# Kernel optimization log

Measured on AMD Instinct MI355X. Metric: run time of the kernel, lower is better.

Reference implementation:

```python
import jax, jax.numpy as jnp
import numpy as np

ITER_N = 5  # Newton-Schulz iterations (SqrtmLayer(cov, 5))


def covpool(x):
    # x: [B, C, M]. MPNCOV CovpoolLayer: x @ I_hat @ x^T with
    # I_hat = (1/M)(I - J/M), a projector, so cov = xc @ xc^T / M.
    M = x.shape[-1]
    xc = x - x.mean(axis=-1, keepdims=True)
    return jnp.einsum('bcm,bdm->bcd', xc, xc) / M


def sqrtm_ns(A, iter_n=ITER_N):
    # MPNCOV SqrtmLayer: trace-normalized Newton-Schulz matrix square root.
    C = A.shape[-1]
    I = jnp.eye(C, dtype=A.dtype)
    normA = jnp.trace(A, axis1=-2, axis2=-1)[:, None, None]  # [B,1,1]
    Y = A / normA
    Z = jnp.broadcast_to(I, A.shape)
    for i in range(iter_n):
        T = 0.5 * (3.0 * I - Z @ Y)
        Y_new = Y @ T
        if i < iter_n - 1:
            Z = T @ Z
        Y = Y_new
    return Y * jnp.sqrt(normA)


def setup_inputs() -> dict:
    key = jax.random.key(0)
    k1, k2, k3 = jax.random.split(key, 3)
    B, C, H, W = 32, 256, 64, 64
    r = 8
    x = jax.random.normal(k1, (B, C, H, W), dtype=jnp.float32)
    w1 = jax.random.normal(k2, (C // r, C), dtype=jnp.float32) * 0.05
    b1 = jnp.zeros((C // r,), dtype=jnp.float32)
    w2 = jax.random.normal(k3, (C, C // r), dtype=jnp.float32) * 0.05
    b2 = jnp.zeros((C,), dtype=jnp.float32)
    return {'x': x, 'w1': w1, 'b1': b1, 'w2': w2, 'b2': b2}


def reference(x, w1, b1, w2, b2):
    B, C, h, w = x.shape
    # h, w < 1000 => x_sub = x (no center crop)
    xf = x.reshape(B, C, h * w)
    cov = covpool(xf)                      # [B, C, C]
    cov_sqrt = sqrtm_ns(cov, ITER_N)       # [B, C, C]
    v = cov_sqrt.mean(axis=1)              # mean over dim 1 -> [B, C]
    # 1x1 convs on a 1x1 map == dense layers
    hdn = jax.nn.relu(jnp.einsum('oc,bc->bo', w1, v) + b1)
    a = jax.nn.sigmoid(jnp.einsum('oc,bc->bo', w2, hdn) + b2)  # [B, C]
    return a[:, :, None, None] * x
```

## Files before the change

kernel.cpp:

```cpp
#include <hip/hip_runtime.h>
#include <hip/hip_bf16.h>

typedef unsigned int uint32;
using short8 = __attribute__((ext_vector_type(8))) short;
using ushort4_t = __attribute__((ext_vector_type(4))) unsigned short;
using f32x4  = __attribute__((ext_vector_type(4))) float;

#define B_ 32
#define C_ 256
#define M_ 4096
#define MATF 2097152

#define AS1 __attribute__((address_space(1)))
#define AS3 __attribute__((address_space(3)))

__device__ inline ushort f2bf(float f) {
  uint32 u = __builtin_bit_cast(uint32, f);
  u += 0x7FFFu + ((u >> 16) & 1u);
  return (ushort)(u >> 16);
}
__device__ inline float bf2f(ushort u) {
  uint32 v = ((uint32)u) << 16;
  return __builtin_bit_cast(float, v);
}
__device__ inline void gl_lds16(const ushort* g, ushort* l) {
  __builtin_amdgcn_global_load_lds((const AS1 void*)g, (AS3 void*)l, 16, 0, 0);
}

__global__ __launch_bounds__(1024)
void covpool_kernel(const float* __restrict__ x, float* __restrict__ parts,
                    float* __restrict__ rs) {
  const int bid = blockIdx.x;
  const int b = bid >> 3, s = bid & 7;
  const int kb = s * 512;
  const float* Xb = x + (size_t)b * C_ * M_;
  float* P = parts + (size_t)s * MATF + ((size_t)b << 16);

  __shared__ ushort As[256 * 64];

  const int t    = threadIdx.x;
  const int lane = t & 63;
  const int w    = t >> 6;
  const int wr   = w >> 2, wc = w & 3;
  const int row  = t >> 2;
  const int ch   = t & 3;

  float rsum = 0.f;
  f32x4 acc[4][4];
#pragma unroll
  for (int m = 0; m < 4; ++m)
#pragma unroll
    for (int n = 0; n < 4; ++n) acc[m][n] = f32x4{0.f, 0.f, 0.f, 0.f};

  const int swzbase = (row & 7) << 4;
  char* wbase = (char*)As + row * 128;

  for (int k0 = kb; k0 < kb + 512; k0 += 64) {
    __syncthreads();
    const float* src = Xb + (size_t)row * M_ + k0 + ch * 16;
    const float4 v0 = ((const float4*)src)[0];
    const float4 v1 = ((const float4*)src)[1];
    const float4 v2 = ((const float4*)src)[2];
    const float4 v3 = ((const float4*)src)[3];
    rsum += v0.x + v0.y + v0.z + v0.w + v1.x + v1.y + v1.z + v1.w +
            v2.x + v2.y + v2.z + v2.w + v3.x + v3.y + v3.z + v3.w;
    short8 h0, h1;
    h0[0] = (short)f2bf(v0.x); h0[1] = (short)f2bf(v0.y);
    h0[2] = (short)f2bf(v0.z); h0[3] = (short)f2bf(v0.w);
    h0[4] = (short)f2bf(v1.x); h0[5] = (short)f2bf(v1.y);
    h0[6] = (short)f2bf(v1.z); h0[7] = (short)f2bf(v1.w);
    h1[0] = (short)f2bf(v2.x); h1[1] = (short)f2bf(v2.y);
    h1[2] = (short)f2bf(v2.z); h1[3] = (short)f2bf(v2.w);
    h1[4] = (short)f2bf(v3.x); h1[5] = (short)f2bf(v3.y);
    h1[6] = (short)f2bf(v3.z); h1[7] = (short)f2bf(v3.w);
    const int c0 = ch * 2;
    *(short8*)(wbase + ((c0 * 16) ^ swzbase))       = h0;
    *(short8*)(wbase + (((c0 + 1) * 16) ^ swzbase)) = h1;
    __syncthreads();
#pragma unroll
    for (int kk = 0; kk < 2; ++kk) {
      short8 af[4], bfr[4];
      const int slot = kk * 4 + (lane >> 4);
#pragma unroll
      for (int m = 0; m < 4; ++m) {
        const int ar = wr * 64 + m * 16 + (lane & 15);
        af[m] = *(const short8*)((const char*)As + ar * 128 + ((slot * 16) ^ ((ar & 7) << 4)));
      }
#pragma unroll
      for (int n = 0; n < 4; ++n) {
        const int br = wc * 64 + n * 16 + (lane & 15);
        bfr[n] = *(const short8*)((const char*)As + br * 128 + ((slot * 16) ^ ((br & 7) << 4)));
      }
#pragma unroll
      for (int m = 0; m < 4; ++m)
#pragma unroll
        for (int n = 0; n < 4; ++n)
          acc[m][n] = __builtin_amdgcn_mfma_f32_16x16x32_bf16(af[m], bfr[n], acc[m][n], 0, 0, 0);
    }
  }

  rsum += __shfl_xor(rsum, 1);
  rsum += __shfl_xor(rsum, 2);
  if (ch == 0) rs[b * 2048 + s * 256 + row] = rsum;

#pragma unroll
  for (int m = 0; m < 4; ++m)
#pragma unroll
    for (int n = 0; n < 4; ++n)
#pragma unroll
      for (int r = 0; r < 4; ++r) {
        const int lr = wr * 64 + m * 16 + ((lane >> 4) * 4) + r;
        const int lc = wc * 64 + n * 16 + (lane & 15);
        P[(size_t)lr * C_ + lc] = acc[m][n][r];
      }
}

__global__ __launch_bounds__(256)
void trace_kernel(const float* __restrict__ parts, const float* __restrict__ rs,
                  float* __restrict__ invn, float* __restrict__ sqrtn) {
  const int b = blockIdx.x;
  const int i = threadIdx.x;
  const float invM = 1.0f / (float)M_;
  float d = 0.f, m = 0.f;
#pragma unroll
  for (int s = 0; s < 8; ++s) {
    d += parts[(size_t)s * MATF + ((size_t)b << 16) + (size_t)i * 257];
    m += rs[b * 2048 + s * 256 + i];
  }
  const float mu = m * invM;
  float v = d * invM - mu * mu;
#pragma unroll
  for (int o = 32; o > 0; o >>= 1) v += __shfl_xor(v, o);
  __shared__ float wsum[4];
  if ((i & 63) == 0) wsum[i >> 6] = v;
  __syncthreads();
  if (i == 0) {
    const float n = wsum[0] + wsum[1] + wsum[2] + wsum[3];
    invn[b]  = 1.0f / n;
    sqrtn[b] = sqrtf(n);
  }
}

__global__ __launch_bounds__(256)
void reduceprep_kernel(const float* __restrict__ parts, const float* __restrict__ rs,
                       const float* __restrict__ invn,
                       ushort* __restrict__ Y0, ushort* __restrict__ Z1) {
  const int idx = blockIdx.x * 256 + threadIdx.x;
  const int b   = idx >> 14;
  const int rem = idx & 16383;
  const int i   = rem >> 6;
  const int j   = (rem & 63) * 4;
  const float invM = 1.0f / (float)M_;
  const float4* p4 = (const float4*)parts;

  float4 g = {0.f, 0.f, 0.f, 0.f};
  float  mi = 0.f;
  float4 mj = {0.f, 0.f, 0.f, 0.f};
#pragma unroll
  for (int s = 0; s < 8; ++s) {
    const float4 gs = p4[(size_t)s * (MATF / 4) + idx];
    g.x += gs.x; g.y += gs.y; g.z += gs.z; g.w += gs.w;
    const float* rrow = rs + b * 2048 + s * 256;
    mi += rrow[i];
    const float4 ms = *(const float4*)(rrow + j);
    mj.x += ms.x; mj.y += ms.y; mj.z += ms.z; mj.w += ms.w;
  }
  mi *= invM;
  const float in = invn[b];
  float y0 = (g.x * invM - mi * (mj.x * invM)) * in;
  float y1 = (g.y * invM - mi * (mj.y * invM)) * in;
  float y2 = (g.z * invM - mi * (mj.z * invM)) * in;
  float y3 = (g.w * invM - mi * (mj.w * invM)) * in;

  ushort4_t yv, zv;
  yv[0] = f2bf(y0); yv[1] = f2bf(y1); yv[2] = f2bf(y2); yv[3] = f2bf(y3);
  zv[0] = f2bf((j + 0 == i ? 1.5f : 0.f) - 0.5f * y0);
  zv[1] = f2bf((j + 1 == i ? 1.5f : 0.f) - 0.5f * y1);
  zv[2] = f2bf((j + 2 == i ? 1.5f : 0.f) - 0.5f * y2);
  zv[3] = f2bf((j + 3 == i ? 1.5f : 0.f) - 0.5f * y3);
  ((ushort4_t*)Y0)[idx] = yv;
  ((ushort4_t*)Z1)[idx] = zv;
}

#define MODE_T 0
#define MODE_W 1
#define MODE_I0 2

template <int MODE>
__global__ __launch_bounds__(256)
void gemm_ns(const ushort* __restrict__ A0, const ushort* __restrict__ A1,
             const ushort* __restrict__ Bm,
             ushort* __restrict__ O0, ushort* __restrict__ O1) {
  const int bid0 = blockIdx.x;
  int bid = (MODE == MODE_W) ? ((bid0 & 7) * 128 + (bid0 >> 3))
                             : ((bid0 & 7) * 64 + (bid0 >> 3));
  const ushort* Aall = A0;
  ushort* Oall = O0;
  if (MODE == MODE_W && bid >= 512) { bid -= 512; Aall = A1; Oall = O1; }
  const int b    = bid >> 4;
  const int tile = bid & 15;
  const int rb   = (tile >> 2) * 64;
  const int cb   = (tile & 3) * 64;
  const ushort* Ap = Aall + ((size_t)b << 16) + rb * C_;
  const ushort* Bp = Bm   + ((size_t)b << 16) + cb * C_;
  ushort* Op = Oall + ((size_t)b << 16);

  __shared__ ushort As[64 * 64];
  __shared__ ushort Bs[64 * 64];

  const int t    = threadIdx.x;
  const int lane = t & 63;
  const int wid  = t >> 6;
  const int wr   = wid >> 1, wc = wid & 1;

  const int srow0 = t >> 3;
  const int sc0   = (t & 7) ^ (srow0 & 7);
  const int srow1 = 32 + srow0;
  const int sc1   = (t & 7) ^ (srow1 & 7);

  f32x4 acc[2][2];
#pragma unroll
  for (int m = 0; m < 2; ++m)
#pragma unroll
    for (int n = 0; n < 2; ++n) acc[m][n] = f32x4{0.f, 0.f, 0.f, 0.f};

  for (int k0 = 0; k0 < C_; k0 += 64) {
    __syncthreads();
    gl_lds16(Ap + (size_t)srow0 * C_ + k0 + sc0 * 8, (ushort*)((char*)As + wid * 1024));
    gl_lds16(Ap + (size_t)srow1 * C_ + k0 + sc1 * 8, (ushort*)((char*)As + 4096 + wid * 1024));
    gl_lds16(Bp + (size_t)srow0 * C_ + k0 + sc0 * 8, (ushort*)((char*)Bs + wid * 1024));
    gl_lds16(Bp + (size_t)srow1 * C_ + k0 + sc1 * 8, (ushort*)((char*)Bs + 4096 + wid * 1024));
    __syncthreads();
#pragma unroll
    for (int kk = 0; kk < 2; ++kk) {
      short8 af[2], bfr[2];
      const int slot = kk * 4 + (lane >> 4);
#pragma unroll
      for (int m = 0; m < 2; ++m) {
        const int ar = wr * 32 + m * 16 + (lane & 15);
        af[m] = *(const short8*)((const char*)As + ar * 128 + ((slot * 16) ^ ((ar & 7) << 4)));
      }
#pragma unroll
      for (int n = 0; n < 2; ++n) {
        const int br = wc * 32 + n * 16 + (lane & 15);
        bfr[n] = *(const short8*)((const char*)Bs + br * 128 + ((slot * 16) ^ ((br & 7) << 4)));
      }
#pragma unroll
      for (int m = 0; m < 2; ++m)
#pragma unroll
        for (int n = 0; n < 2; ++n)
          acc[m][n] = __builtin_amdgcn_mfma_f32_16x16x32_bf16(af[m], bfr[n], acc[m][n], 0, 0, 0);
    }
  }

#pragma unroll
  for (int m = 0; m < 2; ++m)
#pragma unroll
    for (int n = 0; n < 2; ++n)
#pragma unroll
      for (int r = 0; r < 4; ++r) {
        const int lr = wr * 32 + m * 16 + ((lane >> 4) * 4) + r;
        const int lc = wc * 32 + n * 16 + (lane & 15);
        const float v = acc[m][n][r];
        float o;
        if (MODE == MODE_T)       o = (((rb + lr) == (cb + lc)) ? 1.5f : 0.0f) - 0.5f * v;
        else if (MODE == MODE_W)  o = v;
        else         o = 1.5f * bf2f(Ap[lr * C_ + (cb + lc)]) - 0.5f * v;
        Op[(size_t)(rb + lr) * C_ + (cb + lc)] = f2bf(o);
      }
}

__global__ __launch_bounds__(256)
void final_kernel(const ushort* __restrict__ Y, const ushort* __restrict__ T,
                  const float* __restrict__ sqrtn,
                  const float* __restrict__ w1, const float* __restrict__ b1,
                  const float* __restrict__ w2, const float* __restrict__ b2,
                  float* __restrict__ a) {
  const int b = blockIdx.x;
  const int c = threadIdx.x;
  __shared__ float u[C_], vv[C_], h[32];
  const ushort* Yb = Y + ((size_t)b << 16);
  const ushort* Tb = T + ((size_t)b << 16);

  float s = 0.f;
  for (int i = 0; i < C_; ++i) s += bf2f(Yb[(size_t)i * C_ + c]);
  u[c] = s * (1.0f / (float)C_);
  __syncthreads();

  float acc = 0.f;
  for (int k = 0; k < C_; ++k) acc += u[k] * bf2f(Tb[(size_t)k * C_ + c]);
  vv[c] = acc * sqrtn[b];
  __syncthreads();

  if (c < 32) {
    float hh = b1[c];
    for (int k = 0; k < C_; ++k) hh += w1[c * C_ + k] * vv[k];
    h[c] = fmaxf(hh, 0.0f);
  }
  __syncthreads();

  float aa = b2[c];
#pragma unroll
  for (int o = 0; o < 32; ++o) aa += w2[c * 32 + o] * h[o];
  a[b * C_ + c] = 1.0f / (1.0f + expf(-aa));
}

__global__ __launch_bounds__(256)
void scale_kernel(const float* __restrict__ x, const float* __restrict__ a,
                  float* __restrict__ out) {
  const int stride = gridDim.x * blockDim.x;
  const int n4 = B_ * C_ * M_ / 4;
  for (int i = blockIdx.x * blockDim.x + threadIdx.x; i < n4; i += stride) {
    const float4 v = ((const float4*)x)[i];
    const float s = a[i >> 10];
    float4 o = { v.x * s, v.y * s, v.z * s, v.w * s };
    ((float4*)out)[i] = o;
  }
}

extern "C" void kernel_launch(void* const* d_in, const int* in_sizes, int n_in,
                              void* d_out, int out_size, void* d_ws, size_t ws_size,
                              hipStream_t stream) {
  const float* x  = (const float*)d_in[0];
  const float* w1 = (const float*)d_in[1];
  const float* b1 = (const float*)d_in[2];
  const float* w2 = (const float*)d_in[3];
  const float* b2 = (const float*)d_in[4];
  float* out = (float*)d_out;

  float* ws = (float*)d_ws;
  float* parts = ws;
  float* rs    = ws + 8 * (size_t)MATF;
  float* invn  = rs + 65536;
  float* sqrtn = invn + 32;
  float* a     = sqrtn + 32;
  ushort* bfb  = (ushort*)(a + 8192);
  ushort* Yb0  = bfb;
  ushort* Yb1  = bfb + 1 * (size_t)MATF;
  ushort* Zb0  = bfb + 2 * (size_t)MATF;
  ushort* Zb1  = bfb + 3 * (size_t)MATF;
  ushort* Tb   = bfb + 4 * (size_t)MATF;

  covpool_kernel<<<256, 1024, 0, stream>>>(x, parts, rs);
  trace_kernel<<<32, 256, 0, stream>>>(parts, rs, invn, sqrtn);
  reduceprep_kernel<<<2048, 256, 0, stream>>>(parts, rs, invn, Yb0, Zb0);

  gemm_ns<MODE_I0><<<512, 256, 0, stream>>>(Yb0, nullptr, Yb0, Yb1, nullptr);
  gemm_ns<MODE_T><<<512, 256, 0, stream>>>(Zb0, nullptr, Yb1, Tb, nullptr);
  gemm_ns<MODE_W><<<1024, 256, 0, stream>>>(Yb1, Zb0, Tb, Yb0, Zb1);
  gemm_ns<MODE_T><<<512, 256, 0, stream>>>(Zb1, nullptr, Yb0, Tb, nullptr);
  gemm_ns<MODE_W><<<1024, 256, 0, stream>>>(Yb0, Zb1, Tb, Yb1, Zb0);
  gemm_ns<MODE_T><<<512, 256, 0, stream>>>(Zb0, nullptr, Yb1, Tb, nullptr);
  gemm_ns<MODE_W><<<1024, 256, 0, stream>>>(Yb1, Zb0, Tb, Yb0, Zb1);
  gemm_ns<MODE_T><<<512, 256, 0, stream>>>(Zb1, nullptr, Yb0, Tb, nullptr);

  final_kernel<<<32, 256, 0, stream>>>(Yb0, Tb, sqrtn, w1, b1, w2, b2, a);
  scale_kernel<<<4096, 256, 0, stream>>>(x, a, out);
}
```

Baseline: 367.9 us.

## Reformulate Newton-Schulz via commuting polynomial in normalized covariance and mean vector

The Newton-Schulz iteration is rewritten using the fact that Y and Z are polynomials of the normalized covariance A. Only one matrix E_k is updated, E_{k+1} = E_k(1.5I - 0.5E_k^2), through two GEMM launches per step. The column mean is carried as a vector via matrix-vector products fused into the same launches, which removes the separate T, W and Z GEMMs and the associated memory traffic. The change also stores covariance partial sums as bf16 instead of fp32, cutting the split-K reduction traffic, and double-buffers the LDS stages in both the covpool and GEMM kernels. It adds bf16 rounding error on the partial sums and relies on the commuting-polynomial identity staying numerically close to the reference.

```diff
diff --git a/kernel.cpp b/kernel.cpp
--- a/kernel.cpp
+++ b/kernel.cpp
@@ -15,9 +15,8 @@
 #define AS3 __attribute__((address_space(3)))
 
 __device__ inline ushort f2bf(float f) {
-  uint32 u = __builtin_bit_cast(uint32, f);
-  u += 0x7FFFu + ((u >> 16) & 1u);
-  return (ushort)(u >> 16);
+  __hip_bfloat16 h = __float2bfloat16(f);
+  return __builtin_bit_cast(unsigned short, h);
 }
 __device__ inline float bf2f(ushort u) {
   uint32 v = ((uint32)u) << 16;
@@ -28,15 +27,15 @@
 }
 
 __global__ __launch_bounds__(1024)
-void covpool_kernel(const float* __restrict__ x, float* __restrict__ parts,
+void covpool_kernel(const float* __restrict__ x, ushort* __restrict__ parts,
                     float* __restrict__ rs) {
   const int bid = blockIdx.x;
   const int b = bid >> 3, s = bid & 7;
   const int kb = s * 512;
   const float* Xb = x + (size_t)b * C_ * M_;
-  float* P = parts + (size_t)s * MATF + ((size_t)b << 16);
-
-  __shared__ ushort As[256 * 64];
+  ushort* P = parts + (size_t)s * MATF + ((size_t)b << 16);
+
+  __shared__ ushort As[2][256 * 64];
 
   const int t    = threadIdx.x;
   const int lane = t & 63;
@@ -53,30 +52,35 @@
     for (int n = 0; n < 4; ++n) acc[m][n] = f32x4{0.f, 0.f, 0.f, 0.f};
 
   const int swzbase = (row & 7) << 4;
-  char* wbase = (char*)As + row * 128;
-
-  for (int k0 = kb; k0 < kb + 512; k0 += 64) {
+  const float* srcbase = Xb + (size_t)row * M_ + ch * 16;
+
+  float4 cv[4];
+  {
+    const float4* p = (const float4*)(srcbase + kb);
+    cv[0] = p[0]; cv[1] = p[1]; cv[2] = p[2]; cv[3] = p[3];
+  }
+
+#pragma unroll
+  for (int st = 0; st < 8; ++st) {
+    float4 nv[4];
+    if (st < 7) {
+      const float4* p = (const float4*)(srcbase + kb + (st + 1) * 64);
+      nv[0] = p[0]; nv[1] = p[1]; nv[2] = p[2]; nv[3] = p[3];
+    }
+    char* wbase = (char*)As[st & 1] + row * 128;
+#pragma unroll
+    for (int q = 0; q < 2; ++q) {
+      const float4 a = cv[2 * q], bq = cv[2 * q + 1];
+      rsum += a.x + a.y + a.z + a.w + bq.x + bq.y + bq.z + bq.w;
+      short8 h;
+      h[0] = (short)f2bf(a.x);  h[1] = (short)f2bf(a.y);
+      h[2] = (short)f2bf(a.z);  h[3] = (short)f2bf(a.w);
+      h[4] = (short)f2bf(bq.x); h[5] = (short)f2bf(bq.y);
+      h[6] = (short)f2bf(bq.z); h[7] = (short)f2bf(bq.w);
+      *(short8*)(wbase + (((ch * 2 + q) * 16) ^ swzbase)) = h;
+    }
     __syncthreads();
-    const float* src = Xb + (size_t)row * M_ + k0 + ch * 16;
-    const float4 v0 = ((const float4*)src)[0];
-    const float4 v1 = ((const float4*)src)[1];
-    const float4 v2 = ((const float4*)src)[2];
-    const float4 v3 = ((const float4*)src)[3];
-    rsum += v0.x + v0.y + v0.z + v0.w + v1.x + v1.y + v1.z + v1.w +
-            v2.x + v2.y + v2.z + v2.w + v3.x + v3.y + v3.z + v3.w;
-    short8 h0, h1;
-    h0[0] = (short)f2bf(v0.x); h0[1] = (short)f2bf(v0.y);
-    h0[2] = (short)f2bf(v0.z); h0[3] = (short)f2bf(v0.w);
-    h0[4] = (short)f2bf(v1.x); h0[5] = (short)f2bf(v1.y);
-    h0[6] = (short)f2bf(v1.z); h0[7] = (short)f2bf(v1.w);
-    h1[0] = (short)f2bf(v2.x); h1[1] = (short)f2bf(v2.y);
-    h1[2] = (short)f2bf(v2.z); h1[3] = (short)f2bf(v2.w);
-    h1[4] = (short)f2bf(v3.x); h1[5] = (short)f2bf(v3.y);
-    h1[6] = (short)f2bf(v3.z); h1[7] = (short)f2bf(v3.w);
-    const int c0 = ch * 2;
-    *(short8*)(wbase + ((c0 * 16) ^ swzbase))       = h0;
-    *(short8*)(wbase + (((c0 + 1) * 16) ^ swzbase)) = h1;
-    __syncthreads();
+    const char* rb_ = (const char*)As[st & 1];
 #pragma unroll
     for (int kk = 0; kk < 2; ++kk) {
       short8 af[4], bfr[4];
@@ -84,12 +88,12 @@
 #pragma unroll
       for (int m = 0; m < 4; ++m) {
         const int ar = wr * 64 + m * 16 + (lane & 15);
-        af[m] = *(const short8*)((const char*)As + ar * 128 + ((slot * 16) ^ ((ar & 7) << 4)));
+        af[m] = *(const short8*)(rb_ + ar * 128 + ((slot * 16) ^ ((ar & 7) << 4)));
       }
 #pragma unroll
       for (int n = 0; n < 4; ++n) {
         const int br = wc * 64 + n * 16 + (lane & 15);
-        bfr[n] = *(const short8*)((const char*)As + br * 128 + ((slot * 16) ^ ((br & 7) << 4)));
+        bfr[n] = *(const short8*)(rb_ + br * 128 + ((slot * 16) ^ ((br & 7) << 4)));
       }
 #pragma unroll
       for (int m = 0; m < 4; ++m)
@@ -97,6 +101,7 @@
         for (int n = 0; n < 4; ++n)
           acc[m][n] = __builtin_amdgcn_mfma_f32_16x16x32_bf16(af[m], bfr[n], acc[m][n], 0, 0, 0);
     }
+    if (st < 7) { cv[0] = nv[0]; cv[1] = nv[1]; cv[2] = nv[2]; cv[3] = nv[3]; }
   }
 
   rsum += __shfl_xor(rsum, 1);
@@ -111,12 +116,12 @@
       for (int r = 0; r < 4; ++r) {
         const int lr = wr * 64 + m * 16 + ((lane >> 4) * 4) + r;
         const int lc = wc * 64 + n * 16 + (lane & 15);
-        P[(size_t)lr * C_ + lc] = acc[m][n][r];
+        P[(size_t)lr * C_ + lc] = f2bf(acc[m][n][r]);
       }
 }
 
 __global__ __launch_bounds__(256)
-void trace_kernel(const float* __restrict__ parts, const float* __restrict__ rs,
+void trace_kernel(const ushort* __restrict__ parts, const float* __restrict__ rs,
                   float* __restrict__ invn, float* __restrict__ sqrtn) {
   const int b = blockIdx.x;
   const int i = threadIdx.x;
@@ -124,7 +129,7 @@
   float d = 0.f, m = 0.f;
 #pragma unroll
   for (int s = 0; s < 8; ++s) {
-    d += parts[(size_t)s * MATF + ((size_t)b << 16) + (size_t)i * 257];
+    d += bf2f(parts[(size_t)s * MATF + ((size_t)b << 16) + (size_t)i * 257]);
     m += rs[b * 2048 + s * 256 + i];
   }
   const float mu = m * invM;
@@ -142,24 +147,23 @@
 }
 
 __global__ __launch_bounds__(256)
-void reduceprep_kernel(const float* __restrict__ parts, const float* __restrict__ rs,
-                       const float* __restrict__ invn,
-                       ushort* __restrict__ Y0, ushort* __restrict__ Z1) {
+void reduceprep_kernel(const ushort* __restrict__ parts, const float* __restrict__ rs,
+                       const float* __restrict__ invn, ushort* __restrict__ E0) {
   const int idx = blockIdx.x * 256 + threadIdx.x;
   const int b   = idx >> 14;
   const int rem = idx & 16383;
   const int i   = rem >> 6;
   const int j   = (rem & 63) * 4;
   const float invM = 1.0f / (float)M_;
-  const float4* p4 = (const float4*)parts;
-
-  float4 g = {0.f, 0.f, 0.f, 0.f};
-  float  mi = 0.f;
+  const ushort4_t* p4 = (const ushort4_t*)parts;
+
+  float g0 = 0.f, g1 = 0.f, g2 = 0.f, g3 = 0.f;
+  float mi = 0.f;
   float4 mj = {0.f, 0.f, 0.f, 0.f};
 #pragma unroll
   for (int s = 0; s < 8; ++s) {
-    const float4 gs = p4[(size_t)s * (MATF / 4) + idx];
-    g.x += gs.x; g.y += gs.y; g.z += gs.z; g.w += gs.w;
+    const ushort4_t gs = p4[(size_t)s * (MATF / 4) + idx];
+    g0 += bf2f(gs[0]); g1 += bf2f(gs[1]); g2 += bf2f(gs[2]); g3 += bf2f(gs[3]);
     const float* rrow = rs + b * 2048 + s * 256;
     mi += rrow[i];
     const float4 ms = *(const float4*)(rrow + j);
@@ -167,46 +171,45 @@
   }
   mi *= invM;
   const float in = invn[b];
-  float y0 = (g.x * invM - mi * (mj.x * invM)) * in;
-  float y1 = (g.y * invM - mi * (mj.y * invM)) * in;
-  float y2 = (g.z * invM - mi * (mj.z * invM)) * in;
-  float y3 = (g.w * invM - mi * (mj.w * invM)) * in;
-
-  ushort4_t yv, zv;
-  yv[0] = f2bf(y0); yv[1] = f2bf(y1); yv[2] = f2bf(y2); yv[3] = f2bf(y3);
-  zv[0] = f2bf((j + 0 == i ? 1.5f : 0.f) - 0.5f * y0);
-  zv[1] = f2bf((j + 1 == i ? 1.5f : 0.f) - 0.5f * y1);
-  zv[2] = f2bf((j + 2 == i ? 1.5f : 0.f) - 0.5f * y2);
-  zv[3] = f2bf((j + 3 == i ? 1.5f : 0.f) - 0.5f * y3);
-  ((ushort4_t*)Y0)[idx] = yv;
-  ((ushort4_t*)Z1)[idx] = zv;
-}
-
-#define MODE_T 0
-#define MODE_W 1
-#define MODE_I0 2
-
-template <int MODE>
-__global__ __launch_bounds__(256)
-void gemm_ns(const ushort* __restrict__ A0, const ushort* __restrict__ A1,
-             const ushort* __restrict__ Bm,
-             ushort* __restrict__ O0, ushort* __restrict__ O1) {
+  ushort4_t ev;
+  ev[0] = f2bf((g0 * invM - mi * (mj.x * invM)) * in);
+  ev[1] = f2bf((g1 * invM - mi * (mj.y * invM)) * in);
+  ev[2] = f2bf((g2 * invM - mi * (mj.z * invM)) * in);
+  ev[3] = f2bf((g3 * invM - mi * (mj.w * invM)) * in);
+  ((ushort4_t*)E0)[idx] = ev;
+}
+
+template <int MV>
+__global__ __launch_bounds__(256)
+void gemm_i0(const ushort* __restrict__ A, const ushort* __restrict__ B,
+             ushort* __restrict__ O,
+             const float* __restrict__ win, float* __restrict__ wout) {
   const int bid0 = blockIdx.x;
-  int bid = (MODE == MODE_W) ? ((bid0 & 7) * 128 + (bid0 >> 3))
-                             : ((bid0 & 7) * 64 + (bid0 >> 3));
-  const ushort* Aall = A0;
-  ushort* Oall = O0;
-  if (MODE == MODE_W && bid >= 512) { bid -= 512; Aall = A1; Oall = O1; }
+  if (MV && bid0 >= 512) {
+    const int b = bid0 - 512;
+    const int t = threadIdx.x;
+    const ushort* Eb = B + ((size_t)b << 16);
+    __shared__ float wsm[256];
+    wsm[t] = win ? win[b * 256 + t] : (1.0f / 256.0f);
+    __syncthreads();
+    float acc = 0.f;
+#pragma unroll 4
+    for (int k = 0; k < 256; ++k) acc += bf2f(Eb[(size_t)k * 256 + t]) * wsm[k];
+    wout[b * 256 + t] = 1.5f * wsm[t] - 0.5f * acc;
+    return;
+  }
+
+  const int bid = (bid0 & 7) * 64 + (bid0 >> 3);
   const int b    = bid >> 4;
   const int tile = bid & 15;
   const int rb   = (tile >> 2) * 64;
   const int cb   = (tile & 3) * 64;
-  const ushort* Ap = Aall + ((size_t)b << 16) + rb * C_;
-  const ushort* Bp = Bm   + ((size_t)b << 16) + cb * C_;
-  ushort* Op = Oall + ((size_t)b << 16);
-
-  __shared__ ushort As[64 * 64];
-  __shared__ ushort Bs[64 * 64];
+  const ushort* Ap = A + ((size_t)b << 16) + rb * C_;
+  const ushort* Bp = B + ((size_t)b << 16) + cb * C_;
+  ushort* Op = O + ((size_t)b << 16);
+
+  __shared__ ushort As[2][64 * 64];
+  __shared__ ushort Bs[2][64 * 64];
 
   const int t    = threadIdx.x;
   const int lane = t & 63;
@@ -224,34 +227,53 @@
 #pragma unroll
     for (int n = 0; n < 2; ++n) acc[m][n] = f32x4{0.f, 0.f, 0.f, 0.f};
 
-  for (int k0 = 0; k0 < C_; k0 += 64) {
+#define STAGE(k0, c)                                                            \
+  do {                                                                          \
+    gl_lds16(Ap + (size_t)srow0 * C_ + (k0) + sc0 * 8, &As[c][0]    + wid*512); \
+    gl_lds16(Ap + (size_t)srow1 * C_ + (k0) + sc1 * 8, &As[c][2048] + wid*512); \
+    gl_lds16(Bp + (size_t)srow0 * C_ + (k0) + sc0 * 8, &Bs[c][0]    + wid*512); \
+    gl_lds16(Bp + (size_t)srow1 * C_ + (k0) + sc1 * 8, &Bs[c][2048] + wid*512); \
+  } while (0)
+
+#define COMPUTE(c)                                                              \
+  do {                                                                          \
+    const char* ab = (const char*)As[c];                                        \
+    const char* bb = (const char*)Bs[c];                                        \
+    _Pragma("unroll")                                                           \
+    for (int kk = 0; kk < 2; ++kk) {                                            \
+      short8 af[2], bfr[2];                                                     \
+      const int slot = kk * 4 + (lane >> 4);                                    \
+      _Pragma("unroll")                                                         \
+      for (int m = 0; m < 2; ++m) {                                             \
+        const int ar = wr * 32 + m * 16 + (lane & 15);                          \
+        af[m] = *(const short8*)(ab + ar * 128 + ((slot * 16) ^ ((ar & 7) << 4))); \
+      }                                                                         \
+      _Pragma("unroll")                                                         \
+      for (int n = 0; n < 2; ++n) {                                             \
+        const int br = wc * 32 + n * 16 + (lane & 15);                          \
+        bfr[n] = *(const short8*)(bb + br * 128 + ((slot * 16) ^ ((br & 7) << 4))); \
+      }                                                                         \
+      _Pragma("unroll")                                                         \
+      for (int m = 0; m < 2; ++m)                                               \
+        _Pragma("unroll")                                                       \
+        for (int n = 0; n < 2; ++n)                                             \
+          acc[m][n] = __builtin_amdgcn_mfma_f32_16x16x32_bf16(af[m], bfr[n], acc[m][n], 0, 0, 0); \
+    }                                                                           \
+  } while (0)
+
+  STAGE(0, 0);
+  __syncthreads();
+  int cur = 0;
+#pragma unroll
+  for (int k0 = 64; k0 < 256; k0 += 64) {
+    STAGE(k0, cur ^ 1);
+    COMPUTE(cur);
     __syncthreads();
-    gl_lds16(Ap + (size_t)srow0 * C_ + k0 + sc0 * 8, (ushort*)((char*)As + wid * 1024));
-    gl_lds16(Ap + (size_t)srow1 * C_ + k0 + sc1 * 8, (ushort*)((char*)As + 4096 + wid * 1024));
-    gl_lds16(Bp + (size_t)srow0 * C_ + k0 + sc0 * 8, (ushort*)((char*)Bs + wid * 1024));
-    gl_lds16(Bp + (size_t)srow1 * C_ + k0 + sc1 * 8, (ushort*)((char*)Bs + 4096 + wid * 1024));
-    __syncthreads();
-#pragma unroll
-    for (int kk = 0; kk < 2; ++kk) {
-      short8 af[2], bfr[2];
-      const int slot = kk * 4 + (lane >> 4);
-#pragma unroll
-      for (int m = 0; m < 2; ++m) {
-        const int ar = wr * 32 + m * 16 + (lane & 15);
-        af[m] = *(const short8*)((const char*)As + ar * 128 + ((slot * 16) ^ ((ar & 7) << 4)));
-      }
-#pragma unroll
-      for (int n = 0; n < 2; ++n) {
-        const int br = wc * 32 + n * 16 + (lane & 15);
-        bfr[n] = *(const short8*)((const char*)Bs + br * 128 + ((slot * 16) ^ ((br & 7) << 4)));
-      }
-#pragma unroll
-      for (int m = 0; m < 2; ++m)
-#pragma unroll
-        for (int n = 0; n < 2; ++n)
-          acc[m][n] = __builtin_amdgcn_mfma_f32_16x16x32_bf16(af[m], bfr[n], acc[m][n], 0, 0, 0);
-    }
-  }
+    cur ^= 1;
+  }
+  COMPUTE(cur);
+#undef STAGE
+#undef COMPUTE
 
 #pragma unroll
   for (int m = 0; m < 2; ++m)
@@ -261,35 +283,35 @@
       for (int r = 0; r < 4; ++r) {
         const int lr = wr * 32 + m * 16 + ((lane >> 4) * 4) + r;
         const int lc = wc * 32 + n * 16 + (lane & 15);
-        const float v = acc[m][n][r];
-        float o;
-        if (MODE == MODE_T)       o = (((rb + lr) == (cb + lc)) ? 1.5f : 0.0f) - 0.5f * v;
-        else if (MODE == MODE_W)  o = v;
-        else         o = 1.5f * bf2f(Ap[lr * C_ + (cb + lc)]) - 0.5f * v;
+        const float o = 1.5f * bf2f(Ap[lr * C_ + (cb + lc)]) - 0.5f * acc[m][n][r];
         Op[(size_t)(rb + lr) * C_ + (cb + lc)] = f2bf(o);
       }
 }
 
 __global__ __launch_bounds__(256)
-void final_kernel(const ushort* __restrict__ Y, const ushort* __restrict__ T,
-                  const float* __restrict__ sqrtn,
+void final_kernel(const ushort* __restrict__ E4, const ushort* __restrict__ E0,
+                  const float* __restrict__ wvin, const float* __restrict__ sqrtn,
                   const float* __restrict__ w1, const float* __restrict__ b1,
                   const float* __restrict__ w2, const float* __restrict__ b2,
                   float* __restrict__ a) {
   const int b = blockIdx.x;
   const int c = threadIdx.x;
-  __shared__ float u[C_], vv[C_], h[32];
-  const ushort* Yb = Y + ((size_t)b << 16);
-  const ushort* Tb = T + ((size_t)b << 16);
-
-  float s = 0.f;
-  for (int i = 0; i < C_; ++i) s += bf2f(Yb[(size_t)i * C_ + c]);
-  u[c] = s * (1.0f / (float)C_);
-  __syncthreads();
-
+  __shared__ float w4s[C_], w5[C_], vv[C_], h[32];
+  const ushort* E4b = E4 + ((size_t)b << 16);
+  const ushort* E0b = E0 + ((size_t)b << 16);
+
+  w4s[c] = wvin[b * C_ + c];
+  __syncthreads();
   float acc = 0.f;
-  for (int k = 0; k < C_; ++k) acc += u[k] * bf2f(Tb[(size_t)k * C_ + c]);
-  vv[c] = acc * sqrtn[b];
+#pragma unroll 4
+  for (int k = 0; k < C_; ++k) acc += bf2f(E4b[(size_t)k * C_ + c]) * w4s[k];
+  w5[c] = 1.5f * w4s[c] - 0.5f * acc;
+  __syncthreads();
+
+  float acc2 = 0.f;
+#pragma unroll 4
+  for (int k = 0; k < C_; ++k) acc2 += bf2f(E0b[(size_t)k * C_ + c]) * w5[k];
+  vv[c] = acc2 * sqrtn[b];
   __syncthreads();
 
   if (c < 32) {
@@ -329,31 +351,31 @@
   float* out = (float*)d_out;
 
   float* ws = (float*)d_ws;
-  float* parts = ws;
-  float* rs    = ws + 8 * (size_t)MATF;
+  ushort* partsbf = (ushort*)ws;
+  float* rs    = ws + 4 * (size_t)MATF;
   float* invn  = rs + 65536;
   float* sqrtn = invn + 32;
   float* a     = sqrtn + 32;
-  ushort* bfb  = (ushort*)(a + 8192);
-  ushort* Yb0  = bfb;
-  ushort* Yb1  = bfb + 1 * (size_t)MATF;
-  ushort* Zb0  = bfb + 2 * (size_t)MATF;
-  ushort* Zb1  = bfb + 3 * (size_t)MATF;
-  ushort* Tb   = bfb + 4 * (size_t)MATF;
-
-  covpool_kernel<<<256, 1024, 0, stream>>>(x, parts, rs);
-  trace_kernel<<<32, 256, 0, stream>>>(parts, rs, invn, sqrtn);
-  reduceprep_kernel<<<2048, 256, 0, stream>>>(parts, rs, invn, Yb0, Zb0);
-
-  gemm_ns<MODE_I0><<<512, 256, 0, stream>>>(Yb0, nullptr, Yb0, Yb1, nullptr);
-  gemm_ns<MODE_T><<<512, 256, 0, stream>>>(Zb0, nullptr, Yb1, Tb, nullptr);
-  gemm_ns<MODE_W><<<1024, 256, 0, stream>>>(Yb1, Zb0, Tb, Yb0, Zb1);
-  gemm_ns<MODE_T><<<512, 256, 0, stream>>>(Zb1, nullptr, Yb0, Tb, nullptr);
-  gemm_ns<MODE_W><<<1024, 256, 0, stream>>>(Yb0, Zb1, Tb, Yb1, Zb0);
-  gemm_ns<MODE_T><<<512, 256, 0, stream>>>(Zb0, nullptr, Yb1, Tb, nullptr);
-  gemm_ns<MODE_W><<<1024, 256, 0, stream>>>(Yb1, Zb0, Tb, Yb0, Zb1);
-  gemm_ns<MODE_T><<<512, 256, 0, stream>>>(Zb1, nullptr, Yb0, Tb, nullptr);
-
-  final_kernel<<<32, 256, 0, stream>>>(Yb0, Tb, sqrtn, w1, b1, w2, b2, a);
+  float* wvA   = a + 8192;
+  float* wvB   = wvA + 8192;
+  ushort* E0 = (ushort*)(wvB + 8192);
+  ushort* EB = E0 + (size_t)MATF;
+  ushort* EC = EB + (size_t)MATF;
+  ushort* U  = EC + (size_t)MATF;
+
+  covpool_kernel<<<256, 1024, 0, stream>>>(x, partsbf, rs);
+  trace_kernel<<<32, 256, 0, stream>>>(partsbf, rs, invn, sqrtn);
+  reduceprep_kernel<<<2048, 256, 0, stream>>>(partsbf, rs, invn, E0);
+
+  gemm_i0<1><<<544, 256, 0, stream>>>(E0, E0, U, nullptr, wvA);
+  gemm_i0<0><<<512, 256, 0, stream>>>(U, E0, EB, nullptr, nullptr);
+  gemm_i0<1><<<544, 256, 0, stream>>>(EB, EB, U, wvA, wvB);
+  gemm_i0<0><<<512, 256, 0, stream>>>(U, EB, EC, nullptr, nullptr);
+  gemm_i0<1><<<544, 256, 0, stream>>>(EC, EC, U, wvB, wvA);
+  gemm_i0<0><<<512, 256, 0, stream>>>(U, EC, EB, nullptr, nullptr);
+  gemm_i0<1><<<544, 256, 0, stream>>>(EB, EB, U, wvA, wvB);
+  gemm_i0<0><<<512, 256, 0, stream>>>(U, EB, EC, nullptr, nullptr);
+
+  final_kernel<<<32, 256, 0, stream>>>(EC, E0, wvB, sqrtn, w1, b1, w2, b2, a);
   scale_kernel<<<4096, 256, 0, stream>>>(x, a, out);
 }
```

Measured after the change: 445.8 us. 1.21x slower.

## Fuse Newton-Schulz iterations into one per-batch kernel using a symmetric recurrence

Applied to the files above, without the earlier changes.

Replaces the eight separate Y/Z/T GEMM launches and the final kernel with one kernel that runs one block per batch. It tracks a single symmetric matrix iterate and carries the column-mean vector through matrix-vector updates instead of keeping both Y and Z. The GEMMs now load MFMA operands straight from global memory, with no LDS staging. This removes launch overhead and halves the matrix state, but only 32 workgroups do all the matmul work, so GPU utilisation may fall sharply. The bf16 rounding path also changes to the library conversion.

```diff
diff --git a/kernel.cpp b/kernel.cpp
--- a/kernel.cpp
+++ b/kernel.cpp
@@ -11,20 +11,13 @@
 #define M_ 4096
 #define MATF 2097152
 
-#define AS1 __attribute__((address_space(1)))
-#define AS3 __attribute__((address_space(3)))
-
 __device__ inline ushort f2bf(float f) {
-  uint32 u = __builtin_bit_cast(uint32, f);
-  u += 0x7FFFu + ((u >> 16) & 1u);
-  return (ushort)(u >> 16);
+  __hip_bfloat16 h = __float2bfloat16(f);
+  return __builtin_bit_cast(unsigned short, h);
 }
 __device__ inline float bf2f(ushort u) {
   uint32 v = ((uint32)u) << 16;
   return __builtin_bit_cast(float, v);
-}
-__device__ inline void gl_lds16(const ushort* g, ushort* l) {
-  __builtin_amdgcn_global_load_lds((const AS1 void*)g, (AS3 void*)l, 16, 0, 0);
 }
 
 __global__ __launch_bounds__(1024)
@@ -143,8 +136,7 @@
 
 __global__ __launch_bounds__(256)
 void reduceprep_kernel(const float* __restrict__ parts, const float* __restrict__ rs,
-                       const float* __restrict__ invn,
-                       ushort* __restrict__ Y0, ushort* __restrict__ Z1) {
+                       const float* __restrict__ invn, ushort* __restrict__ E0) {
   const int idx = blockIdx.x * 256 + threadIdx.x;
   const int b   = idx >> 14;
   const int rem = idx & 16383;
@@ -167,142 +159,138 @@
   }
   mi *= invM;
   const float in = invn[b];
-  float y0 = (g.x * invM - mi * (mj.x * invM)) * in;
-  float y1 = (g.y * invM - mi * (mj.y * invM)) * in;
-  float y2 = (g.z * invM - mi * (mj.z * invM)) * in;
-  float y3 = (g.w * invM - mi * (mj.w * invM)) * in;
-
-  ushort4_t yv, zv;
-  yv[0] = f2bf(y0); yv[1] = f2bf(y1); yv[2] = f2bf(y2); yv[3] = f2bf(y3);
-  zv[0] = f2bf((j + 0 == i ? 1.5f : 0.f) - 0.5f * y0);
-  zv[1] = f2bf((j + 1 == i ? 1.5f : 0.f) - 0.5f * y1);
-  zv[2] = f2bf((j + 2 == i ? 1.5f : 0.f) - 0.5f * y2);
-  zv[3] = f2bf((j + 3 == i ? 1.5f : 0.f) - 0.5f * y3);
-  ((ushort4_t*)Y0)[idx] = yv;
-  ((ushort4_t*)Z1)[idx] = zv;
-}
-
-#define MODE_T 0
-#define MODE_W 1
-#define MODE_I0 2
-
-template <int MODE>
-__global__ __launch_bounds__(256)
-void gemm_ns(const ushort* __restrict__ A0, const ushort* __restrict__ A1,
-             const ushort* __restrict__ Bm,
-             ushort* __restrict__ O0, ushort* __restrict__ O1) {
-  const int bid0 = blockIdx.x;
-  int bid = (MODE == MODE_W) ? ((bid0 & 7) * 128 + (bid0 >> 3))
-                             : ((bid0 & 7) * 64 + (bid0 >> 3));
-  const ushort* Aall = A0;
-  ushort* Oall = O0;
-  if (MODE == MODE_W && bid >= 512) { bid -= 512; Aall = A1; Oall = O1; }
-  const int b    = bid >> 4;
-  const int tile = bid & 15;
-  const int rb   = (tile >> 2) * 64;
-  const int cb   = (tile & 3) * 64;
-  const ushort* Ap = Aall + ((size_t)b << 16) + rb * C_;
-  const ushort* Bp = Bm   + ((size_t)b << 16) + cb * C_;
-  ushort* Op = Oall + ((size_t)b << 16);
-
-  __shared__ ushort As[64 * 64];
-  __shared__ ushort Bs[64 * 64];
+  ushort4_t ev;
+  ev[0] = f2bf((g.x * invM - mi * (mj.x * invM)) * in);
+  ev[1] = f2bf((g.y * invM - mi * (mj.y * invM)) * in);
+  ev[2] = f2bf((g.z * invM - mi * (mj.z * invM)) * in);
+  ev[3] = f2bf((g.w * invM - mi * (mj.w * invM)) * in);
+  ((ushort4_t*)E0)[idx] = ev;
+}
+
+__device__ __forceinline__ void mm_unit(const ushort* __restrict__ Ap,
+                                        const ushort* __restrict__ Bp,
+                                        ushort* __restrict__ Op,
+                                        int R, int Cc, int lane) {
+  f32x4 acc[4][4];
+#pragma unroll
+  for (int m = 0; m < 4; ++m)
+#pragma unroll
+    for (int n = 0; n < 4; ++n) acc[m][n] = f32x4{0.f, 0.f, 0.f, 0.f};
+
+#pragma unroll 1
+  for (int ks = 0; ks < 8; ++ks) {
+    const int ko = ks * 32 + (lane >> 4) * 8;
+    short8 af[4], bfm[4];
+#pragma unroll
+    for (int m = 0; m < 4; ++m)
+      af[m] = *(const short8*)(Ap + (size_t)(R + m * 16 + (lane & 15)) * 256 + ko);
+#pragma unroll
+    for (int n = 0; n < 4; ++n)
+      bfm[n] = *(const short8*)(Bp + (size_t)(Cc + n * 16 + (lane & 15)) * 256 + ko);
+#pragma unroll
+    for (int m = 0; m < 4; ++m)
+#pragma unroll
+      for (int n = 0; n < 4; ++n)
+        acc[m][n] = __builtin_amdgcn_mfma_f32_16x16x32_bf16(af[m], bfm[n], acc[m][n], 0, 0, 0);
+  }
+
+#pragma unroll
+  for (int m = 0; m < 4; ++m)
+#pragma unroll
+    for (int n = 0; n < 4; ++n)
+#pragma unroll
+      for (int r = 0; r < 4; ++r) {
+        const int lr = R + m * 16 + ((lane >> 4) * 4) + r;
+        const int lc = Cc + n * 16 + (lane & 15);
+        const float o = 1.5f * bf2f(Ap[(size_t)lr * 256 + lc]) - 0.5f * acc[m][n][r];
+        Op[(size_t)lr * 256 + lc] = f2bf(o);
+      }
+}
+
+__global__ __launch_bounds__(1024)
+void ns_kernel(const ushort* __restrict__ E0g, ushort* __restrict__ Eag,
+               ushort* __restrict__ Ebg, ushort* __restrict__ Ug,
+               const float* __restrict__ sqrtn,
+               const float* __restrict__ w1, const float* __restrict__ b1,
+               const float* __restrict__ w2, const float* __restrict__ b2,
+               float* __restrict__ a) {
+  const int b = blockIdx.x;
+  const size_t off = (size_t)b << 16;
+  const ushort* E0 = E0g + off;
+  ushort* Ea = Eag + off;
+  ushort* Eb = Ebg + off;
+  ushort* U  = Ug  + off;
 
   const int t    = threadIdx.x;
   const int lane = t & 63;
-  const int wid  = t >> 6;
-  const int wr   = wid >> 1, wc = wid & 1;
-
-  const int srow0 = t >> 3;
-  const int sc0   = (t & 7) ^ (srow0 & 7);
-  const int srow1 = 32 + srow0;
-  const int sc1   = (t & 7) ^ (srow1 & 7);
-
-  f32x4 acc[2][2];
-#pragma unroll
-  for (int m = 0; m < 2; ++m)
-#pragma unroll
-    for (int n = 0; n < 2; ++n) acc[m][n] = f32x4{0.f, 0.f, 0.f, 0.f};
-
-  for (int k0 = 0; k0 < C_; k0 += 64) {
+  const int w    = t >> 6;
+  const int R    = (w >> 2) * 64;
+  const int Cc   = (w & 3) * 64;
+  const int c    = t & 255;
+  const int q    = t >> 8;
+
+  __shared__ float wv[2][C_];
+  __shared__ float pw[4][C_];
+  __shared__ float vv[C_];
+  __shared__ float hh[32];
+
+  if (t < C_) { wv[0][t] = 1.0f / (float)C_; }
+  __syncthreads();
+
+  const ushort* Ecur = E0;
+  int p = 0;
+#pragma unroll 1
+  for (int k = 0; k < 5; ++k) {
+    {
+      float part = 0.f;
+      const int k0 = q * 64;
+#pragma unroll 8
+      for (int kk = 0; kk < 64; ++kk)
+        part += bf2f(Ecur[(size_t)(k0 + kk) * C_ + c]) * wv[p][k0 + kk];
+      pw[q][c] = part;
+      __syncthreads();
+      if (t < C_) {
+        const float s = pw[0][t] + pw[1][t] + pw[2][t] + pw[3][t];
+        wv[p ^ 1][t] = 1.5f * wv[p][t] - 0.5f * s;
+      }
+      __syncthreads();
+      p ^= 1;
+    }
+    if (k < 4) {
+      mm_unit(Ecur, Ecur, U, R, Cc, lane);
+      __syncthreads();
+      ushort* Enext = (k & 1) ? Eb : Ea;
+      mm_unit(U, Ecur, Enext, R, Cc, lane);
+      __syncthreads();
+      Ecur = Enext;
+    }
+  }
+
+  {
+    float part = 0.f;
+    const int k0 = q * 64;
+#pragma unroll 8
+    for (int kk = 0; kk < 64; ++kk)
+      part += bf2f(E0[(size_t)(k0 + kk) * C_ + c]) * wv[p][k0 + kk];
+    pw[q][c] = part;
     __syncthreads();
-    gl_lds16(Ap + (size_t)srow0 * C_ + k0 + sc0 * 8, (ushort*)((char*)As + wid * 1024));
-    gl_lds16(Ap + (size_t)srow1 * C_ + k0 + sc1 * 8, (ushort*)((char*)As + 4096 + wid * 1024));
-    gl_lds16(Bp + (size_t)srow0 * C_ + k0 + sc0 * 8, (ushort*)((char*)Bs + wid * 1024));
-    gl_lds16(Bp + (size_t)srow1 * C_ + k0 + sc1 * 8, (ushort*)((char*)Bs + 4096 + wid * 1024));
+    if (t < C_)
+      vv[t] = (pw[0][t] + pw[1][t] + pw[2][t] + pw[3][t]) * sqrtn[b];
     __syncthreads();
-#pragma unroll
-    for (int kk = 0; kk < 2; ++kk) {
-      short8 af[2], bfr[2];
-      const int slot = kk * 4 + (lane >> 4);
-#pragma unroll
-      for (int m = 0; m < 2; ++m) {
-        const int ar = wr * 32 + m * 16 + (lane & 15);
-        af[m] = *(const short8*)((const char*)As + ar * 128 + ((slot * 16) ^ ((ar & 7) << 4)));
-      }
-#pragma unroll
-      for (int n = 0; n < 2; ++n) {
-        const int br = wc * 32 + n * 16 + (lane & 15);
-        bfr[n] = *(const short8*)((const char*)Bs + br * 128 + ((slot * 16) ^ ((br & 7) << 4)));
-      }
-#pragma unroll
-      for (int m = 0; m < 2; ++m)
-#pragma unroll
-        for (int n = 0; n < 2; ++n)
-          acc[m][n] = __builtin_amdgcn_mfma_f32_16x16x32_bf16(af[m], bfr[n], acc[m][n], 0, 0, 0);
-    }
-  }
-
-#pragma unroll
-  for (int m = 0; m < 2; ++m)
-#pragma unroll
-    for (int n = 0; n < 2; ++n)
-#pragma unroll
-      for (int r = 0; r < 4; ++r) {
-        const int lr = wr * 32 + m * 16 + ((lane >> 4) * 4) + r;
-        const int lc = wc * 32 + n * 16 + (lane & 15);
-        const float v = acc[m][n][r];
-        float o;
-        if (MODE == MODE_T)       o = (((rb + lr) == (cb + lc)) ? 1.5f : 0.0f) - 0.5f * v;
-        else if (MODE == MODE_W)  o = v;
-        else         o = 1.5f * bf2f(Ap[lr * C_ + (cb + lc)]) - 0.5f * v;
-        Op[(size_t)(rb + lr) * C_ + (cb + lc)] = f2bf(o);
-      }
-}
-
-__global__ __launch_bounds__(256)
-void final_kernel(const ushort* __restrict__ Y, const ushort* __restrict__ T,
-                  const float* __restrict__ sqrtn,
-                  const float* __restrict__ w1, const float* __restrict__ b1,
-                  const float* __restrict__ w2, const float* __restrict__ b2,
-                  float* __restrict__ a) {
-  const int b = blockIdx.x;
-  const int c = threadIdx.x;
-  __shared__ float u[C_], vv[C_], h[32];
-  const ushort* Yb = Y + ((size_t)b << 16);
-  const ushort* Tb = T + ((size_t)b << 16);
-
-  float s = 0.f;
-  for (int i = 0; i < C_; ++i) s += bf2f(Yb[(size_t)i * C_ + c]);
-  u[c] = s * (1.0f / (float)C_);
+  }
+
+  if (t < 32) {
+    float h = b1[t];
+    for (int k = 0; k < C_; ++k) h += w1[t * C_ + k] * vv[k];
+    hh[t] = fmaxf(h, 0.0f);
+  }
   __syncthreads();
-
-  float acc = 0.f;
-  for (int k = 0; k < C_; ++k) acc += u[k] * bf2f(Tb[(size_t)k * C_ + c]);
-  vv[c] = acc * sqrtn[b];
-  __syncthreads();
-
-  if (c < 32) {
-    float hh = b1[c];
-    for (int k = 0; k < C_; ++k) hh += w1[c * C_ + k] * vv[k];
-    h[c] = fmaxf(hh, 0.0f);
-  }
-  __syncthreads();
-
-  float aa = b2[c];
-#pragma unroll
-  for (int o = 0; o < 32; ++o) aa += w2[c * 32 + o] * h[o];
-  a[b * C_ + c] = 1.0f / (1.0f + expf(-aa));
+  if (t < C_) {
+    float aa = b2[t];
+#pragma unroll
+    for (int o = 0; o < 32; ++o) aa += w2[t * 32 + o] * hh[o];
+    a[b * C_ + t] = 1.0f / (1.0f + expf(-aa));
+  }
 }
 
 __global__ __launch_bounds__(256)
@@ -334,26 +322,14 @@
   float* invn  = rs + 65536;
   float* sqrtn = invn + 32;
   float* a     = sqrtn + 32;
-  ushort* bfb  = (ushort*)(a + 8192);
-  ushort* Yb0  = bfb;
-  ushort* Yb1  = bfb + 1 * (size_t)MATF;
-  ushort* Zb0  = bfb + 2 * (size_t)MATF;
-  ushort* Zb1  = bfb + 3 * (size_t)MATF;
-  ushort* Tb   = bfb + 4 * (size_t)MATF;
+  ushort* E0 = (ushort*)(a + 8192);
+  ushort* Ea = E0 + (size_t)MATF;
+  ushort* Eb = Ea + (size_t)MATF;
+  ushort* U  = Eb + (size_t)MATF;
 
   covpool_kernel<<<256, 1024, 0, stream>>>(x, parts, rs);
   trace_kernel<<<32, 256, 0, stream>>>(parts, rs, invn, sqrtn);
-  reduceprep_kernel<<<2048, 256, 0, stream>>>(parts, rs, invn, Yb0, Zb0);
-
-  gemm_ns<MODE_I0><<<512, 256, 0, stream>>>(Yb0, nullptr, Yb0, Yb1, nullptr);
-  gemm_ns<MODE_T><<<512, 256, 0, stream>>>(Zb0, nullptr, Yb1, Tb, nullptr);
-  gemm_ns<MODE_W><<<1024, 256, 0, stream>>>(Yb1, Zb0, Tb, Yb0, Zb1);
-  gemm_ns<MODE_T><<<512, 256, 0, stream>>>(Zb1, nullptr, Yb0, Tb, nullptr);
-  gemm_ns<MODE_W><<<1024, 256, 0, stream>>>(Yb0, Zb1, Tb, Yb1, Zb0);
-  gemm_ns<MODE_T><<<512, 256, 0, stream>>>(Zb0, nullptr, Yb1, Tb, nullptr);
-  gemm_ns<MODE_W><<<1024, 256, 0, stream>>>(Yb1, Zb0, Tb, Yb0, Zb1);
-  gemm_ns<MODE_T><<<512, 256, 0, stream>>>(Zb1, nullptr, Yb0, Tb, nullptr);
-
-  final_kernel<<<32, 256, 0, stream>>>(Yb0, Tb, sqrtn, w1, b1, w2, b2, a);
+  reduceprep_kernel<<<2048, 256, 0, stream>>>(parts, rs, invn, E0);
+  ns_kernel<<<32, 1024, 0, stream>>>(E0, Ea, Eb, U, sqrtn, w1, b1, w2, b2, a);
   scale_kernel<<<4096, 256, 0, stream>>>(x, a, out);
 }
```

New measurement: 880.0 us. 139% more time.
